# Kernel optimization log

Hardware: AMD Instinct MI355X
Metric: run time of the kernel (lower is better)

The kernel has to match this reference:

```python
import jax, jax.numpy as jnp
import numpy as np

B, S, D, H = 2, 2048, 1024, 16
HD = D // H
SCALE = HD ** -0.5
EPS = 1e-5


def setup_inputs() -> dict:
    key = jax.random.key(0)
    ks = jax.random.split(key, 12)
    s = 1.0 / np.sqrt(D)
    return {
        "query": jax.random.normal(ks[0], (B, S, D), jnp.float32),
        "key_": jax.random.normal(ks[1], (B, S, D), jnp.float32),
        "value": jax.random.normal(ks[2], (B, S, D), jnp.float32),
        "Wq": jax.random.normal(ks[3], (D, D), jnp.float32) * s,
        "bq": jnp.zeros((D,), jnp.float32),
        "Wk": jax.random.normal(ks[4], (D, D), jnp.float32) * s,
        "bk": jnp.zeros((D,), jnp.float32),
        "Wv": jax.random.normal(ks[5], (D, D), jnp.float32) * s,
        "bv": jnp.zeros((D,), jnp.float32),
        "Wo": jax.random.normal(ks[6], (D, D), jnp.float32) * s,
        "bo": jnp.zeros((D,), jnp.float32),
        "gamma": jnp.ones((D,), jnp.float32),
        "beta": jnp.zeros((D,), jnp.float32),
    }


def _split_heads(x):
    # [B,S,D] -> [B,H,S,HD]
    return x.reshape(B, S, H, HD).transpose(0, 2, 1, 3)


def reference(query, key_, value, Wq, bq, Wk, bk, Wv, bv, Wo, bo, gamma, beta):
    q = _split_heads(query @ Wq + bq)
    k = _split_heads(key_ @ Wk + bk)
    v = _split_heads(value @ Wv + bv)
    # [B,H,S,S] attention scores
    scores = jnp.einsum("bhqd,bhkd->bhqk", q, k) * SCALE
    probs = jax.nn.softmax(scores, axis=-1)  # dropout is identity in eval
    attn = jnp.einsum("bhqk,bhkd->bhqd", probs, v)
    attn = attn.transpose(0, 2, 1, 3).reshape(B, S, D)
    attn = attn @ Wo + bo
    # residual + LayerNorm
    x = query + attn
    mu = jnp.mean(x, axis=-1, keepdims=True)
    var = jnp.mean(jnp.square(x - mu), axis=-1, keepdims=True)
    out = (x - mu) * jax.lax.rsqrt(var + EPS) * gamma + beta
    return out
```

## Files before the change

kernel.cpp:

```cpp
#include <hip/hip_runtime.h>
#include <hip/hip_bf16.h>

#define DEVI __device__ __forceinline__

constexpr int Bb  = 2;
constexpr int Ss  = 2048;
constexpr int Dd  = 1024;
constexpr int Hh  = 16;
constexpr int HDh = 64;
constexpr int Mr  = Bb * Ss;
constexpr float kEps = 1e-5f;
constexpr float kQScale = 0.18033688011112043f;

typedef unsigned short u16;
typedef unsigned int   u32;
typedef u16 u16x8 __attribute__((ext_vector_type(8)));
typedef u16 u16x4 __attribute__((ext_vector_type(4)));
typedef __attribute__((ext_vector_type(8)))  short s16x8;
typedef __attribute__((ext_vector_type(16))) float f32x16;
typedef __attribute__((ext_vector_type(4)))  u32   u32x4;

DEVI float bf2f(u16 u) {
  return __builtin_bit_cast(float, ((unsigned int)u) << 16);
}
DEVI u16 f2bf(float f) {
  unsigned int x = __builtin_bit_cast(unsigned int, f);
  return (u16)((x + 0x7FFFu + ((x >> 16) & 1u)) >> 16);
}
DEVI u32 cvt_pk_bf16(float a, float b) {
  u32 r;
  asm("v_cvt_pk_bf16_f32 %0, %1, %2" : "=v"(r) : "v"(a), "v"(b));
  return r;
}
DEVI float vexp2(float x) {
  float r;
  asm("v_exp_f32 %0, %1" : "=v"(r) : "v"(x));
  return r;
}

DEVI void gload_lds16(const void* g, void* l) {
  __builtin_amdgcn_global_load_lds(
      (const __attribute__((address_space(1))) unsigned int*)(unsigned long long)(size_t)g,
      (__attribute__((address_space(3))) unsigned int*)(unsigned int)(size_t)l,
      16, 0, 0);
}


__global__ __launch_bounds__(256) void pack_all_fm(
    const float* __restrict__ X0, const float* __restrict__ X1,
    const float* __restrict__ X2,
    const float* __restrict__ W0, const float* __restrict__ W1,
    const float* __restrict__ W2, const float* __restrict__ W3,
    u16* __restrict__ Y0, u16* __restrict__ Y1, u16* __restrict__ Y2,
    u16* __restrict__ WfmBase) {
  __shared__ u16 Tl[64 * 64];
  const int t   = threadIdx.x;
  const int gid = blockIdx.x;
  if (gid < 3072) {
    const int z   = gid >> 10;
    const int rem = gid & 1023;
    const int r0  = (rem >> 4) * 64, k0 = (rem & 15) * 64;
    const float* X = z == 0 ? X0 : z == 1 ? X1 : X2;
    u16*         Y = z == 0 ? Y0 : z == 1 ? Y1 : Y2;
#pragma unroll
    for (int i = 0; i < 4; ++i) {
      const int idx = t + i * 256;
      const int r = idx >> 4, c4 = (idx & 15) << 2;
      const float4 v = *(const float4*)(X + (size_t)(r0 + r) * 1024 + k0 + c4);
      u16x4 p;
      p[0] = f2bf(v.x); p[1] = f2bf(v.y); p[2] = f2bf(v.z); p[3] = f2bf(v.w);
      *(u16x4*)&Tl[r * 64 + (c4 ^ (8 * (r & 7)))] = p;
    }
    __syncthreads();
#pragma unroll
    for (int i = 0; i < 2; ++i) {
      const int slot = t + i * 256;
      const int f = slot >> 6, l = slot & 63;
      const int l31 = l & 31, g2 = l >> 5;
      const int r = (f >> 2) * 32 + l31;
      const int c = (f & 3) * 16 + g2 * 8;
      const u16x8 v = *(const u16x8*)&Tl[r * 64 + (c ^ (8 * (r & 7)))];
      const size_t t32 = (size_t)(r0 >> 5) + (f >> 2);
      const int s = (k0 >> 4) + (f & 3);
      *(u16x8*)(Y + (t32 * 64 + s) * 512 + l * 8) = v;
    }
  } else {
    const int wz  = (gid - 3072) >> 8;
    const int rem = (gid - 3072) & 255;
    const int n0  = (rem >> 4) * 64, k0 = (rem & 15) * 64;
    const float* W = wz == 0 ? W0 : wz == 1 ? W1 : wz == 2 ? W2 : W3;
    u16* out = WfmBase + (size_t)wz * 1024 * 1024;
#pragma unroll
    for (int i = 0; i < 4; ++i) {
      const int idx = t + i * 256;
      const int r = idx >> 4, c4 = (idx & 15) << 2;
      const float4 v = *(const float4*)(W + (size_t)(k0 + r) * 1024 + n0 + c4);
      u16x4 p;
      p[0] = f2bf(v.x); p[1] = f2bf(v.y); p[2] = f2bf(v.z); p[3] = f2bf(v.w);
      *(u16x4*)&Tl[r * 64 + (c4 ^ (8 * (r & 7)))] = p;
    }
    __syncthreads();
#pragma unroll
    for (int i = 0; i < 2; ++i) {
      const int slot = t + i * 256;
      const int f = slot >> 6, l = slot & 63;
      const int l31 = l & 31, g2 = l >> 5;
      const int rbase = (f & 3) * 16 + g2 * 8;
      const int c = (f >> 2) * 32 + l31;
      u16x8 o;
#pragma unroll
      for (int j = 0; j < 8; ++j) {
        const int r = rbase + j;
        o[j] = Tl[r * 64 + (((c & ~3) ^ (8 * (r & 7))) | (c & 3))];
      }
      const size_t n32 = (size_t)(n0 >> 5) + (f >> 2);
      const int s = (k0 >> 4) + (f & 3);
      *(u16x8*)(out + (n32 * 64 + s) * 512 + l * 8) = o;
    }
  }
}

template <int MODE>
__global__ __launch_bounds__(256, 2) void gemm_reg_k(
    const u16* __restrict__ A0, const u16* __restrict__ A1,
    const u16* __restrict__ Wt0, const u16* __restrict__ Wt1,
    const float* b0, const float* b1, void* C0, void* C1,
    float e0, float e1) {
  constexpr int K = 1024, N = 1024;
  const int z = blockIdx.z;
  const u16*   A    = z ? A1 : A0;
  const u16*   Wt   = z ? Wt1 : Wt0;
  const float* bias = z ? b1 : b0;
  void*        Cv   = z ? C1 : C0;
  const float  esc  = z ? e1 : e0;

  const int t = threadIdx.x;
  const int lane = t & 63, w = t >> 6;
  const int l31 = lane & 31, g2 = lane >> 5;
  const int id  = blockIdx.y * 8 + blockIdx.x;
  const int sid = (id & 7) * 32 + (id >> 3);
  const int m0 = (sid >> 3) * 128, n0 = (sid & 7) * 128;
  const int wr = w >> 1, wc = w & 1;

  const u16* a0p = A  + ((size_t)(m0 >> 5) + 2 * wr) * 32768 + lane * 8;
  const u16* a1p = a0p + 32768;
  const u16* w0p = Wt + ((size_t)(n0 >> 5) + 2 * wc) * 32768 + lane * 8;
  const u16* w1p = w0p + 32768;

  f32x16 acc00, acc01, acc10, acc11;
#pragma unroll
  for (int r = 0; r < 16; ++r) { acc00[r] = 0.f; acc01[r] = 0.f; acc10[r] = 0.f; acc11[r] = 0.f; }

  s16x8 X[8], Y[8], Z[8];
  auto loadset = [&](s16x8* R, int k0) {
    const int o = (k0 >> 4) * 512;
    R[0] = *(const s16x8*)(a0p + o);  R[1] = *(const s16x8*)(a0p + o + 512);
    R[2] = *(const s16x8*)(a1p + o);  R[3] = *(const s16x8*)(a1p + o + 512);
    R[4] = *(const s16x8*)(w0p + o);  R[5] = *(const s16x8*)(w0p + o + 512);
    R[6] = *(const s16x8*)(w1p + o);  R[7] = *(const s16x8*)(w1p + o + 512);
  };
  auto compute = [&](const s16x8* R) {
#pragma unroll
    for (int s = 0; s < 2; ++s) {
      if constexpr (MODE == 1) {
        acc00 = __builtin_amdgcn_mfma_f32_32x32x16_bf16(R[0 + s], R[4 + s], acc00, 0, 0, 0);
        acc01 = __builtin_amdgcn_mfma_f32_32x32x16_bf16(R[0 + s], R[6 + s], acc01, 0, 0, 0);
        acc10 = __builtin_amdgcn_mfma_f32_32x32x16_bf16(R[2 + s], R[4 + s], acc10, 0, 0, 0);
        acc11 = __builtin_amdgcn_mfma_f32_32x32x16_bf16(R[2 + s], R[6 + s], acc11, 0, 0, 0);
      } else {
        acc00 = __builtin_amdgcn_mfma_f32_32x32x16_bf16(R[4 + s], R[0 + s], acc00, 0, 0, 0);
        acc01 = __builtin_amdgcn_mfma_f32_32x32x16_bf16(R[4 + s], R[2 + s], acc01, 0, 0, 0);
        acc10 = __builtin_amdgcn_mfma_f32_32x32x16_bf16(R[6 + s], R[0 + s], acc10, 0, 0, 0);
        acc11 = __builtin_amdgcn_mfma_f32_32x32x16_bf16(R[6 + s], R[2 + s], acc11, 0, 0, 0);
      }
    }
  };

  loadset(X, 0); loadset(Y, 32); loadset(Z, 64);
  int k = 0;
  for (int it = 0; it < 9; ++it, k += 96) {
    compute(X); loadset(X, k + 96);
    compute(Y); loadset(Y, k + 128);
    compute(Z); loadset(Z, k + 160);
  }
  compute(X); loadset(X, 960);
  compute(Y); loadset(Y, 992);
  compute(Z);
  compute(X);
  compute(Y);

  if constexpr (MODE == 1) {
    auto storeVfm = [&](const f32x16& a, int i, int j) {
      const int nn = n0 + (2 * wc + j) * 32 + l31;
      const float bn = bias[nn];
      const int nnT = (n0 >> 5) + 2 * wc + j;
      const int sb  = ((m0 & 2047) + (2 * wr + i) * 32) >> 4;
      u16* vbase = (u16*)Cv + (size_t)(m0 >> 11) * (1024 * 2048);
#pragma unroll
      for (int c = 0; c < 4; ++c) {
        u16x4 o;
#pragma unroll
        for (int rr = 0; rr < 4; ++rr) o[rr] = f2bf(a[4 * c + rr] + bn);
        u16* dst = vbase + ((size_t)nnT * 128 + sb + (c >> 1)) * 512 +
                   (l31 + 32 * (c & 1)) * 8 + 4 * g2;
        *(u16x4*)dst = o;
      }
    };
    storeVfm(acc00, 0, 0); storeVfm(acc01, 0, 1); storeVfm(acc10, 1, 0); storeVfm(acc11, 1, 1);
  } else {
    auto storeRow = [&](const f32x16& a, int i, int j) {
      const int m = m0 + (2 * wr + j) * 32 + l31;
#pragma unroll
      for (int c = 0; c < 4; ++c) {
        const int nb = n0 + (2 * wc + i) * 32 + 8 * c + 4 * g2;
        const float4 b4 = *(const float4*)&bias[nb];
        u16x4 o;
        o[0] = f2bf((a[4 * c + 0] + b4.x) * esc); o[1] = f2bf((a[4 * c + 1] + b4.y) * esc);
        o[2] = f2bf((a[4 * c + 2] + b4.z) * esc); o[3] = f2bf((a[4 * c + 3] + b4.w) * esc);
        *(u16x4*)((u16*)Cv + (size_t)m * N + nb) = o;
      }
    };
    auto storeKfm = [&](const f32x16& a, int i, int j) {
      const int mt = (m0 >> 5) + 2 * wr + j;
#pragma unroll
      for (int c = 0; c < 4; ++c) {
        const int nb = n0 + (2 * wc + i) * 32 + 8 * c + 4 * g2;
        const float4 b4 = *(const float4*)&bias[nb];
        u16x4 o;
        o[0] = f2bf(a[4 * c + 0] + b4.x); o[1] = f2bf(a[4 * c + 1] + b4.y);
        o[2] = f2bf(a[4 * c + 2] + b4.z); o[3] = f2bf(a[4 * c + 3] + b4.w);
        const int nq = (n0 >> 4) + (2 * wc + i) * 2 + (c >> 1);
        u16* dst = (u16*)Cv + ((size_t)mt * 64 + nq) * 512 +
                   (l31 + 32 * (c & 1)) * 8 + 4 * g2;
        *(u16x4*)dst = o;
      }
    };
    if (MODE == 2 && z == 1) {
      storeKfm(acc00, 0, 0); storeKfm(acc01, 0, 1); storeKfm(acc10, 1, 0); storeKfm(acc11, 1, 1);
    } else {
      storeRow(acc00, 0, 0); storeRow(acc01, 0, 1); storeRow(acc10, 1, 0); storeRow(acc11, 1, 1);
    }
  }
}

__global__ __launch_bounds__(256, 2) void flash_mfma_k(
    const u16* __restrict__ Qb, const u16* __restrict__ Kf,
    const u16* __restrict__ Vf, u16* __restrict__ Ofm) {
  __shared__ u16 smem[24576];
  const int t    = threadIdx.x;
  const int lane = t & 63;
  const int w    = t >> 6;
  const int l31  = lane & 31, g2 = lane >> 5;
  const int hid = (blockIdx.z * 16 + blockIdx.y) * 16 + blockIdx.x;
  const int sid = (hid & 7) * 64 + (hid >> 3);
  const int h = (sid >> 4) & 15, b = sid >> 8;
  const int q0 = (sid & 15) * 128 + w * 32;

  s16x8 qf0, qf1, qf2, qf3;
  {
    const u16* qp = Qb + ((size_t)(b * Ss + q0 + l31)) * Dd + h * HDh + 8 * g2;
    qf0 = *(const s16x8*)(qp);
    qf1 = *(const s16x8*)(qp + 16);
    qf2 = *(const s16x8*)(qp + 32);
    qf3 = *(const s16x8*)(qp + 48);
  }

  f32x16 accO0, accO1, zacc;
#pragma unroll
  for (int r = 0; r < 16; ++r) { accO0[r] = 0.f; accO1[r] = 0.f; zacc[r] = 0.f; }
  float l_run = 0.f;

  const int f0 = 2 * w, f1 = 2 * w + 1;
  const u16* kg0 = Kf + (((size_t)b * 64 + (f0 >> 2)) * 64 + h * 4 + (f0 & 3)) * 512 + lane * 8;
  const u16* kg1 = Kf + (((size_t)b * 64 + (f1 >> 2)) * 64 + h * 4 + (f1 & 3)) * 512 + lane * 8;
  const u16* vg0 = Vf + (size_t)b * 2097152 + (((size_t)h * 2 + (f0 >> 2)) * 128 + (f0 & 3)) * 512 + lane * 8;
  const u16* vg1 = Vf + (size_t)b * 2097152 + (((size_t)h * 2 + (f1 >> 2)) * 128 + (f1 & 3)) * 512 + lane * 8;

  auto stage = [&](int buf, int kt) {
    u16* base = &smem[buf * 8192];
    gload_lds16(kg0 + (size_t)kt * 65536, base + f0 * 512);
    gload_lds16(kg1 + (size_t)kt * 65536, base + f1 * 512);
    gload_lds16(vg0 + (size_t)kt * 2048, base + 4096 + f0 * 512);
    gload_lds16(vg1 + (size_t)kt * 2048, base + 4096 + f1 * 512);
  };

  stage(0, 0);
  stage(1, 1);

  int bi = 0;
  for (int i = 0; i < 32; ++i) {
    if (i < 31) asm volatile("s_waitcnt vmcnt(4)" ::: "memory");
    else        asm volatile("s_waitcnt vmcnt(0)" ::: "memory");
    __builtin_amdgcn_s_barrier();
    if (i + 2 < 32) {
      int sbuf = bi + 2; if (sbuf >= 3) sbuf -= 3;
      stage(sbuf, i + 2);
    }
    const u16* sb = &smem[bi * 8192];
    const int lb = lane * 8;

    f32x16 sc0, sc1;
    __builtin_amdgcn_s_setprio(1);
    {
      s16x8 ka;
      ka  = *(const s16x8*)&sb[(0 * 4 + 0) * 512 + lb];
      sc0 = __builtin_amdgcn_mfma_f32_32x32x16_bf16(ka, qf0, zacc, 0, 0, 0);
      ka  = *(const s16x8*)&sb[(0 * 4 + 1) * 512 + lb];
      sc0 = __builtin_amdgcn_mfma_f32_32x32x16_bf16(ka, qf1, sc0, 0, 0, 0);
      ka  = *(const s16x8*)&sb[(0 * 4 + 2) * 512 + lb];
      sc0 = __builtin_amdgcn_mfma_f32_32x32x16_bf16(ka, qf2, sc0, 0, 0, 0);
      ka  = *(const s16x8*)&sb[(0 * 4 + 3) * 512 + lb];
      sc0 = __builtin_amdgcn_mfma_f32_32x32x16_bf16(ka, qf3, sc0, 0, 0, 0);
    }
    __builtin_amdgcn_s_setprio(0);

    float lp = 0.f;
    u32 pw0[4][2];
#pragma unroll
    for (int c = 0; c < 4; ++c) {
      const float e0 = vexp2(sc0[4 * c + 0]);
      const float e1 = vexp2(sc0[4 * c + 1]);
      const float e2 = vexp2(sc0[4 * c + 2]);
      const float e3 = vexp2(sc0[4 * c + 3]);
      lp += (e0 + e1) + (e2 + e3);
      pw0[c][0] = cvt_pk_bf16(e0, e1);
      pw0[c][1] = cvt_pk_bf16(e2, e3);
    }

    __builtin_amdgcn_s_setprio(1);
    {
      s16x8 kb2;
      kb2 = *(const s16x8*)&sb[(1 * 4 + 0) * 512 + lb];
      sc1 = __builtin_amdgcn_mfma_f32_32x32x16_bf16(kb2, qf0, zacc, 0, 0, 0);
      kb2 = *(const s16x8*)&sb[(1 * 4 + 1) * 512 + lb];
      sc1 = __builtin_amdgcn_mfma_f32_32x32x16_bf16(kb2, qf1, sc1, 0, 0, 0);
      kb2 = *(const s16x8*)&sb[(1 * 4 + 2) * 512 + lb];
      sc1 = __builtin_amdgcn_mfma_f32_32x32x16_bf16(kb2, qf2, sc1, 0, 0, 0);
      kb2 = *(const s16x8*)&sb[(1 * 4 + 3) * 512 + lb];
      sc1 = __builtin_amdgcn_mfma_f32_32x32x16_bf16(kb2, qf3, sc1, 0, 0, 0);
    }
    __builtin_amdgcn_s_setprio(0);

#pragma unroll
    for (int s = 0; s < 2; ++s) {
      const int cb = 2 * (s & 1);
      u32 A0w = pw0[cb][0], B0w = pw0[cb + 1][0];
      u32 A1w = pw0[cb][1], B1w = pw0[cb + 1][1];
      asm("v_permlane32_swap_b32 %0, %1" : "+v"(A0w), "+v"(B0w));
      asm("v_permlane32_swap_b32 %0, %1" : "+v"(A1w), "+v"(B1w));
      u32x4 pv;
      pv[0] = A0w; pv[1] = A1w; pv[2] = B0w; pv[3] = B1w;
      const s16x8 pf = __builtin_bit_cast(s16x8, pv);
      const s16x8 v0 = *(const s16x8*)&sb[4096 + (0 * 4 + s) * 512 + lb];
      const s16x8 v1 = *(const s16x8*)&sb[4096 + (1 * 4 + s) * 512 + lb];
      __builtin_amdgcn_s_setprio(1);
      accO0 = __builtin_amdgcn_mfma_f32_32x32x16_bf16(v0, pf, accO0, 0, 0, 0);
      accO1 = __builtin_amdgcn_mfma_f32_32x32x16_bf16(v1, pf, accO1, 0, 0, 0);
      __builtin_amdgcn_s_setprio(0);
    }

    u32 pw1[4][2];
#pragma unroll
    for (int c = 0; c < 4; ++c) {
      const float e0 = vexp2(sc1[4 * c + 0]);
      const float e1 = vexp2(sc1[4 * c + 1]);
      const float e2 = vexp2(sc1[4 * c + 2]);
      const float e3 = vexp2(sc1[4 * c + 3]);
      lp += (e0 + e1) + (e2 + e3);
      pw1[c][0] = cvt_pk_bf16(e0, e1);
      pw1[c][1] = cvt_pk_bf16(e2, e3);
    }
    l_run += lp;

#pragma unroll
    for (int s = 2; s < 4; ++s) {
      const int cb = 2 * (s & 1);
      u32 A0w = pw1[cb][0], B0w = pw1[cb + 1][0];
      u32 A1w = pw1[cb][1], B1w = pw1[cb + 1][1];
      asm("v_permlane32_swap_b32 %0, %1" : "+v"(A0w), "+v"(B0w));
      asm("v_permlane32_swap_b32 %0, %1" : "+v"(A1w), "+v"(B1w));
      u32x4 pv;
      pv[0] = A0w; pv[1] = A1w; pv[2] = B0w; pv[3] = B1w;
      const s16x8 pf = __builtin_bit_cast(s16x8, pv);
      const s16x8 v0 = *(const s16x8*)&sb[4096 + (0 * 4 + s) * 512 + lb];
      const s16x8 v1 = *(const s16x8*)&sb[4096 + (1 * 4 + s) * 512 + lb];
      __builtin_amdgcn_s_setprio(1);
      accO0 = __builtin_amdgcn_mfma_f32_32x32x16_bf16(v0, pf, accO0, 0, 0, 0);
      accO1 = __builtin_amdgcn_mfma_f32_32x32x16_bf16(v1, pf, accO1, 0, 0, 0);
      __builtin_amdgcn_s_setprio(0);
    }

    bi = (bi == 2) ? 0 : bi + 1;
  }

  __syncthreads();

  const float l_tot = l_run + __shfl_xor(l_run, 32);
  const float inv = 1.f / l_tot;
  u16* Ol = &smem[w * 2304];
#pragma unroll
  for (int c = 0; c < 4; ++c) {
    u16x4 pk;
#pragma unroll
    for (int rr = 0; rr < 4; ++rr) pk[rr] = f2bf(accO0[4 * c + rr] * inv);
    *(u16x4*)&Ol[l31 * 72 + 0 * 32 + c * 8 + g2 * 4] = pk;
#pragma unroll
    for (int rr = 0; rr < 4; ++rr) pk[rr] = f2bf(accO1[4 * c + rr] * inv);
    *(u16x4*)&Ol[l31 * 72 + 1 * 32 + c * 8 + g2 * 4] = pk;
  }
  const size_t m32 = (size_t)((b * Ss + q0) >> 5);
#pragma unroll
  for (int s = 0; s < 4; ++s) {
    const u16x8 vv = *(const u16x8*)&Ol[l31 * 72 + s * 16 + g2 * 8];
    *(u16x8*)(Ofm + (m32 * 64 + h * 4 + s) * 512 + lane * 8) = vv;
  }
}

__global__ __launch_bounds__(256) void resid_ln_k(const float* __restrict__ x0,
                                                  const u16* __restrict__ x1,
                                                  const float* __restrict__ gamma,
                                                  const float* __restrict__ beta,
                                                  float* __restrict__ out) {
  const int row = blockIdx.x;
  const int t   = threadIdx.x;
  const size_t base = (size_t)row * Dd + t * 4;
  const float4 a = *(const float4*)(x0 + base);
  const u16x4  c = *(const u16x4*)(x1 + base);
  float x[4] = {a.x + bf2f(c[0]), a.y + bf2f(c[1]), a.z + bf2f(c[2]), a.w + bf2f(c[3])};
  float s  = (x[0] + x[1]) + (x[2] + x[3]);
  float s2 = fmaf(x[0], x[0], fmaf(x[1], x[1], fmaf(x[2], x[2], x[3] * x[3])));
#pragma unroll
  for (int m = 1; m < 64; m <<= 1) {
    s  += __shfl_xor(s, m);
    s2 += __shfl_xor(s2, m);
  }
  __shared__ float red[8];
  const int wave = t >> 6;
  if ((t & 63) == 0) {
    red[wave]     = s;
    red[wave + 4] = s2;
  }
  __syncthreads();
  s  = (red[0] + red[1]) + (red[2] + red[3]);
  s2 = (red[4] + red[5]) + (red[6] + red[7]);
  const float mu  = s * (1.f / Dd);
  const float var = s2 * (1.f / Dd) - mu * mu;
  const float rs  = rsqrtf(var + kEps);
  const float4 g  = *(const float4*)(gamma + t * 4);
  const float4 be = *(const float4*)(beta + t * 4);
  float4 o;
  o.x = (x[0] - mu) * rs * g.x + be.x;
  o.y = (x[1] - mu) * rs * g.y + be.y;
  o.z = (x[2] - mu) * rs * g.z + be.z;
  o.w = (x[3] - mu) * rs * g.w + be.w;
  *(float4*)(out + base) = o;
}

extern "C" void kernel_launch(void* const* d_in, const int* in_sizes, int n_in,
                              void* d_out, int out_size, void* d_ws,
                              size_t ws_size, hipStream_t stream) {
  const float* query = (const float*)d_in[0];
  const float* key_  = (const float*)d_in[1];
  const float* value = (const float*)d_in[2];
  const float* Wq = (const float*)d_in[3];
  const float* bq = (const float*)d_in[4];
  const float* Wk = (const float*)d_in[5];
  const float* bk = (const float*)d_in[6];
  const float* Wv = (const float*)d_in[7];
  const float* bv = (const float*)d_in[8];
  const float* Wo = (const float*)d_in[9];
  const float* bo = (const float*)d_in[10];
  const float* gamma = (const float*)d_in[11];
  const float* beta  = (const float*)d_in[12];
  float* out = (float*)d_out;

  char* ws = (char*)d_ws;
  u16* Xv  = (u16*)(ws + (size_t)0);
  u16* Qb  = (u16*)(ws + (size_t)0);
  u16* Kf  = (u16*)(ws + (size_t)8 * 1024 * 1024);
  u16* XoB = (u16*)(ws + (size_t)8 * 1024 * 1024);
  u16* Vf  = (u16*)(ws + (size_t)16 * 1024 * 1024);
  u16* WfB = (u16*)(ws + (size_t)24 * 1024 * 1024);
  u16* Wqf = WfB;
  u16* Wkf = WfB + (size_t)1 * 1024 * 1024;
  u16* Wvf = WfB + (size_t)2 * 1024 * 1024;
  u16* Wof = WfB + (size_t)3 * 1024 * 1024;
  u16* Xq  = (u16*)d_out;
  u16* Xk  = (u16*)d_out + (size_t)Mr * Dd;
  u16* Ofm = (u16*)d_out;

  pack_all_fm<<<4096, 256, 0, stream>>>(query, key_, value, Wq, Wk, Wv, Wo,
                                        Xq, Xk, Xv, WfB);
  gemm_reg_k<1><<<dim3(8, 32, 1), 256, 0, stream>>>(
      Xv, Xv, Wvf, Wvf, bv, bv, Vf, Vf, 1.f, 1.f);
  gemm_reg_k<2><<<dim3(8, 32, 2), 256, 0, stream>>>(
      Xq, Xk, Wqf, Wkf, bq, bk, Qb, Kf, kQScale, 1.f);
  flash_mfma_k<<<dim3(16, 16, 2), 256, 0, stream>>>(Qb, Kf, Vf, Ofm);
  gemm_reg_k<0><<<dim3(8, 32, 1), 256, 0, stream>>>(
      Ofm, Ofm, Wof, Wof, bo, bo, XoB, XoB, 1.f, 1.f);
  resid_ln_k<<<Mr, 256, 0, stream>>>(query, XoB, gamma, beta, out);
}
```

Before: 125.6 us.

## Restructure flash attention KV pipeline into double-buffered pairs of tiles

Replaces the three-slot single-tile ring buffer with two slots that each hold a pair of K/V tiles, so each barrier covers two tiles of compute. The goal is to halve the number of wait/barrier points per loop and give larger prefetch batches. The cost is more LDS (64KB per block), which may cut occupancy below two blocks per CU, and an extra barrier before refilling a slot. Prefetch distance in tiles stays about the same.

```diff
diff --git a/kernel.cpp b/kernel.cpp
--- a/kernel.cpp
+++ b/kernel.cpp
@@ -246,7 +246,7 @@
 __global__ __launch_bounds__(256, 2) void flash_mfma_k(
     const u16* __restrict__ Qb, const u16* __restrict__ Kf,
     const u16* __restrict__ Vf, u16* __restrict__ Ofm) {
-  __shared__ u16 smem[24576];
+  __shared__ u16 smem[32768];
   const int t    = threadIdx.x;
   const int lane = t & 63;
   const int w    = t >> 6;
@@ -276,29 +276,19 @@
   const u16* vg0 = Vf + (size_t)b * 2097152 + (((size_t)h * 2 + (f0 >> 2)) * 128 + (f0 & 3)) * 512 + lane * 8;
   const u16* vg1 = Vf + (size_t)b * 2097152 + (((size_t)h * 2 + (f1 >> 2)) * 128 + (f1 & 3)) * 512 + lane * 8;
 
-  auto stage = [&](int buf, int kt) {
-    u16* base = &smem[buf * 8192];
-    gload_lds16(kg0 + (size_t)kt * 65536, base + f0 * 512);
-    gload_lds16(kg1 + (size_t)kt * 65536, base + f1 * 512);
-    gload_lds16(vg0 + (size_t)kt * 2048, base + 4096 + f0 * 512);
-    gload_lds16(vg1 + (size_t)kt * 2048, base + 4096 + f1 * 512);
+  auto stage_pair = [&](int pb, int kt) {
+#pragma unroll
+    for (int j = 0; j < 2; ++j) {
+      u16* base = &smem[pb * 16384 + j * 8192];
+      gload_lds16(kg0 + (size_t)(kt + j) * 65536, base + f0 * 512);
+      gload_lds16(kg1 + (size_t)(kt + j) * 65536, base + f1 * 512);
+      gload_lds16(vg0 + (size_t)(kt + j) * 2048, base + 4096 + f0 * 512);
+      gload_lds16(vg1 + (size_t)(kt + j) * 2048, base + 4096 + f1 * 512);
+    }
   };
 
-  stage(0, 0);
-  stage(1, 1);
-
-  int bi = 0;
-  for (int i = 0; i < 32; ++i) {
-    if (i < 31) asm volatile("s_waitcnt vmcnt(4)" ::: "memory");
-    else        asm volatile("s_waitcnt vmcnt(0)" ::: "memory");
-    __builtin_amdgcn_s_barrier();
-    if (i + 2 < 32) {
-      int sbuf = bi + 2; if (sbuf >= 3) sbuf -= 3;
-      stage(sbuf, i + 2);
-    }
-    const u16* sb = &smem[bi * 8192];
+  auto tile_compute = [&](const u16* sb) {
     const int lb = lane * 8;
-
     f32x16 sc0, sc1;
     __builtin_amdgcn_s_setprio(1);
     {
@@ -389,8 +379,22 @@
       accO1 = __builtin_amdgcn_mfma_f32_32x32x16_bf16(v1, pf, accO1, 0, 0, 0);
       __builtin_amdgcn_s_setprio(0);
     }
-
-    bi = (bi == 2) ? 0 : bi + 1;
+  };
+
+  stage_pair(0, 0);
+  stage_pair(1, 2);
+
+  for (int i = 0; i < 16; ++i) {
+    const int pb = i & 1;
+    if (i < 15) asm volatile("s_waitcnt vmcnt(8)" ::: "memory");
+    else        asm volatile("s_waitcnt vmcnt(0)" ::: "memory");
+    __builtin_amdgcn_s_barrier();
+    tile_compute(&smem[pb * 16384]);
+    tile_compute(&smem[pb * 16384 + 8192]);
+    if (i <= 13) {
+      __builtin_amdgcn_s_barrier();
+      stage_pair(pb, 2 * (i + 2));
+    }
   }
 
   __syncthreads();
```

After: 125.2 us. No clear change (-0.3%).
